# Kernel tuning notes

Hardware: AMD Instinct MI355X
Metric: run time of the kernel (lower is better)

Reference implementation:

```python
import jax, jax.numpy as jnp
import numpy as np

B, S, H, OUT, STEPS = 64, 1024, 512, 256, 32


def setup_inputs() -> dict:
    key = jax.random.key(0)
    ks = jax.random.split(key, 10)
    s = 0.02
    return {
        "encoder_outputs": jax.random.normal(ks[0], (B, S, H), jnp.float32),
        "hidden": jax.random.normal(ks[1], (B, H), jnp.float32),
        # Attention: nn.Linear(2H, 1)
        "attn_w": jax.random.normal(ks[2], (2 * H,), jnp.float32) * s,
        "attn_b": jax.random.normal(ks[3], (1,), jnp.float32) * s,
        # LSTMCell(OUT + H, H): torch gate order i, f, g, o
        "w_ih": jax.random.normal(ks[4], (4 * H, OUT + H), jnp.float32) * s,
        "w_hh": jax.random.normal(ks[5], (4 * H, H), jnp.float32) * s,
        "b_ih": jax.random.normal(ks[6], (4 * H,), jnp.float32) * s,
        "b_hh": jax.random.normal(ks[7], (4 * H,), jnp.float32) * s,
        # fc: nn.Linear(H, OUT)
        "fc_w": jax.random.normal(ks[8], (OUT, H), jnp.float32) * s,
        "fc_b": jax.random.normal(ks[9], (OUT,), jnp.float32) * s,
    }


def reference(encoder_outputs, hidden, attn_w, attn_b, w_ih, w_hh, b_ih, b_hh, fc_w, fc_b):
    # Split attention weight: Linear(concat(enc, hid)) == enc@wa_e + hid@wa_d + b
    wa_e, wa_d = attn_w[:H], attn_w[H:]
    # encoder contribution to attention energy is step-invariant: [B, S]
    enc_energy = jnp.einsum("bsh,h->bs", encoder_outputs, wa_e) + attn_b[0]
    bias = b_ih + b_hh  # [4H]

    def step(carry, _):
        h, c, dec_in = carry
        # Bahdanau-style energy and context
        energy = enc_energy + (h @ wa_d)[:, None]          # [B, S]
        weights = jax.nn.softmax(energy, axis=1)
        context = jnp.einsum("bs,bsh->bh", weights, encoder_outputs)
        # LSTMCell (torch gate order i, f, g, o)
        x = jnp.concatenate([dec_in, context], axis=1)     # [B, OUT+H]
        gates = x @ w_ih.T + h @ w_hh.T + bias             # [B, 4H]
        i, f, g, o = jnp.split(gates, 4, axis=1)
        c_new = jax.nn.sigmoid(f) * c + jax.nn.sigmoid(i) * jnp.tanh(g)
        h_new = jax.nn.sigmoid(o) * jnp.tanh(c_new)
        dec_new = h_new @ fc_w.T + fc_b                    # [B, OUT]
        return (h_new, c_new, dec_new), dec_new

    dec0 = jnp.zeros((encoder_outputs.shape[0], fc_w.shape[0]), encoder_outputs.dtype)
    c0 = jnp.zeros_like(hidden)
    _, outs = jax.lax.scan(step, (hidden, c0, dec0), None, length=STEPS)
    return jnp.transpose(outs, (1, 0, 2))  # [B, STEPS, OUT]
```

## Files before the change

### kernel.cpp

```cpp
#include <hip/hip_runtime.h>
#include <math.h>

#define B 64
#define S 1024
#define H 512
#define OUT 256
#define STEPS 32
#define NG 2048
#define X 768

typedef __attribute__((ext_vector_type(8))) short short8;
typedef __attribute__((ext_vector_type(4))) short s16x4;
typedef __attribute__((ext_vector_type(4))) float f32x4;
typedef __attribute__((ext_vector_type(4))) unsigned u32x4;

__device__ __forceinline__ float sigf(float x) { return 1.0f / (1.0f + __expf(-x)); }
__device__ __forceinline__ float tanhf_fast(float x) {
  return 2.0f / (1.0f + __expf(-2.0f * x)) - 1.0f;
}

__device__ __forceinline__ short f2bf(float x) {
  union { float f; unsigned u; } a; a.f = x;
  unsigned r = a.u + 0x7fffu + ((a.u >> 16) & 1u);
  return (short)(r >> 16);
}
__device__ __forceinline__ float bf2f(short s) {
  union { unsigned u; float f; } a; a.u = ((unsigned)(unsigned short)s) << 16;
  return a.f;
}

__device__ __forceinline__ unsigned load_u32_cg(const unsigned* p) {
  unsigned r;
  asm volatile("global_load_dword %0, %1, off sc0 sc1\n\ts_waitcnt vmcnt(0)"
               : "=v"(r) : "v"(p) : "memory");
  return r;
}

__global__ __launch_bounds__(256) void k_pre(
    const float* __restrict__ enc, const float* __restrict__ attn_w,
    float* __restrict__ part_ctx, float* __restrict__ part_ml,
    const float* __restrict__ w_ih, const float* __restrict__ w_hh,
    const float* __restrict__ fc_w, short* __restrict__ whi,
    short* __restrict__ wlo) {
  __shared__ float smem[10336];
  const int cid = blockIdx.x;
  const int tid = threadIdx.x;
  if (cid < 512) {
    float* sm_acc = smem;
    float* sm_m = smem + 2048;
    float* sm_l = smem + 2052;
    const int b = cid >> 3, chunk = cid & 7;
    const int wave = tid >> 6, lane = tid & 63;
    const float4 wa0 = *(const float4*)(attn_w + lane * 8);
    const float4 wa1 = *(const float4*)(attn_w + lane * 8 + 4);
    const float* eb = enc + (long)b * S * H;
    float m = -1e30f, l = 0.0f;
    float acc[8];
#pragma unroll
    for (int r = 0; r < 8; ++r) acc[r] = 0.0f;
    for (int i = 0; i < 32; ++i) {
      const int s = chunk * 128 + i * 4 + wave;
      const float* row = eb + (long)s * H + lane * 8;
      const float4 v0 = *(const float4*)row;
      const float4 v1 = *(const float4*)(row + 4);
      float e = v0.x * wa0.x + v0.y * wa0.y + v0.z * wa0.z + v0.w * wa0.w +
                v1.x * wa1.x + v1.y * wa1.y + v1.z * wa1.z + v1.w * wa1.w;
#pragma unroll
      for (int msk = 1; msk < 64; msk <<= 1) e += __shfl_xor(e, msk, 64);
      const float mn = fmaxf(m, e);
      const float sc = __expf(m - mn);
      const float p = __expf(e - mn);
      l = l * sc + p;
      m = mn;
      acc[0] = acc[0] * sc + p * v0.x; acc[1] = acc[1] * sc + p * v0.y;
      acc[2] = acc[2] * sc + p * v0.z; acc[3] = acc[3] * sc + p * v0.w;
      acc[4] = acc[4] * sc + p * v1.x; acc[5] = acc[5] * sc + p * v1.y;
      acc[6] = acc[6] * sc + p * v1.z; acc[7] = acc[7] * sc + p * v1.w;
    }
#pragma unroll
    for (int r = 0; r < 8; ++r) sm_acc[wave * 512 + lane * 8 + r] = acc[r];
    if (lane == 0) { sm_m[wave] = m; sm_l[wave] = l; }
    __syncthreads();
    const float mb = fmaxf(fmaxf(sm_m[0], sm_m[1]), fmaxf(sm_m[2], sm_m[3]));
    float e0[4];
#pragma unroll
    for (int w = 0; w < 4; ++w) e0[w] = __expf(sm_m[w] - mb);
    const int h0 = tid * 2;
    float s0 = 0.f, s1 = 0.f;
#pragma unroll
    for (int w = 0; w < 4; ++w) {
      s0 += sm_acc[w * 512 + h0] * e0[w];
      s1 += sm_acc[w * 512 + h0 + 1] * e0[w];
    }
    float* pc = part_ctx + ((long)chunk * B + b) * H;
    pc[h0] = s0; pc[h0 + 1] = s1;
    if (tid == 0) {
      const float lb = sm_l[0] * e0[0] + sm_l[1] * e0[1] + sm_l[2] * e0[2] + sm_l[3] * e0[3];
      part_ml[(chunk * B + b) * 2] = mb;
      part_ml[(chunk * B + b) * 2 + 1] = lb;
    }
  } else {
    float* ft = smem;
    float* wd = smem + 8256;
    const int n0 = (cid - 512) * 8;
    for (int i = tid; i < 512; i += 256) {
      const int r = i >> 6, c4 = (i & 63) << 2;
      *(float4*)&wd[r * 260 + c4] = *(const float4*)(w_ih + (long)(n0 + r) * X + c4);
    }
    float acc[16];
#pragma unroll
    for (int e = 0; e < 16; ++e) acc[e] = 0.f;
    const int n_l = tid >> 5, kq = tid & 31;
    for (int jt = 0; jt < 16; ++jt) {
      __syncthreads();
      for (int i = tid; i < 2048; i += 256) {
        const int r = i >> 7, c4 = (i & 127) << 2;
        *(float4*)&ft[r * 516 + c4] =
            *(const float4*)(fc_w + (long)(jt * 16 + r) * H + c4);
      }
      __syncthreads();
#pragma unroll 4
      for (int j = 0; j < 16; ++j) {
        const float w = wd[n_l * 260 + jt * 16 + j];
#pragma unroll
        for (int e4 = 0; e4 < 4; ++e4) {
          const float4 f = *(float4*)&ft[j * 516 + kq * 4 + e4 * 128];
          acc[e4 * 4 + 0] = fmaf(w, f.x, acc[e4 * 4 + 0]);
          acc[e4 * 4 + 1] = fmaf(w, f.y, acc[e4 * 4 + 1]);
          acc[e4 * 4 + 2] = fmaf(w, f.z, acc[e4 * 4 + 2]);
          acc[e4 * 4 + 3] = fmaf(w, f.w, acc[e4 * 4 + 3]);
        }
      }
    }
    const long rbase = (long)(n0 + n_l) * H;
#pragma unroll
    for (int e4 = 0; e4 < 4; ++e4) {
      const int k = kq * 4 + e4 * 128;
      const float4 hh = *(const float4*)(w_hh + rbase + k);
      float v[4] = {acc[e4 * 4] + hh.x, acc[e4 * 4 + 1] + hh.y,
                    acc[e4 * 4 + 2] + hh.z, acc[e4 * 4 + 3] + hh.w};
      s16x4 hi4, lo4;
#pragma unroll
      for (int e = 0; e < 4; ++e) {
        const short hb = f2bf(v[e]);
        hi4[e] = hb;
        lo4[e] = f2bf(v[e] - bf2f(hb));
      }
      *(s16x4*)(whi + rbase + k) = hi4;
      *(s16x4*)(wlo + rbase + k) = lo4;
    }
  }
}

__global__ __launch_bounds__(256) void k_gbase(
    const float* __restrict__ w_ih, const float* __restrict__ w_hh,
    const float* __restrict__ b_ih, const float* __restrict__ b_hh,
    const float* __restrict__ fc_b, const float* __restrict__ part_ctx,
    const float* __restrict__ part_ml, const float* __restrict__ hidden,
    float* __restrict__ gates0, float* __restrict__ gbase2) {
  __shared__ float wt[128][33];
  __shared__ float rb[16][524];
  __shared__ float sfc[256];
  __shared__ float sf[16][8];
  const int n0 = blockIdx.x * 32, b0 = blockIdx.y * 16;
  const int tid = threadIdx.x;
  const int n_l = tid & 31, bh = tid >> 5;
  const int n = n0 + n_l;

  if (tid < 16) {
    const int r = tid;
    float ml[8], ll[8];
    float m = -1e30f;
#pragma unroll
    for (int c = 0; c < 8; ++c) {
      ml[c] = part_ml[(c * B + b0 + r) * 2];
      ll[c] = part_ml[(c * B + b0 + r) * 2 + 1];
      m = fmaxf(m, ml[c]);
    }
    float L = 0.f;
#pragma unroll
    for (int c = 0; c < 8; ++c) L += ll[c] * __expf(ml[c] - m);
    const float inv = 1.0f / L;
#pragma unroll
    for (int c = 0; c < 8; ++c) sf[r][c] = __expf(ml[c] - m) * inv;
  }
  sfc[tid] = fc_b[tid];
  __syncthreads();

  for (int i = tid; i < 16 * 128; i += 256) {
    const int r = i >> 7, c4 = (i & 127) << 2;
    float4 s = {0.f, 0.f, 0.f, 0.f};
#pragma unroll
    for (int c8 = 0; c8 < 8; ++c8) {
      const float4 p = *(const float4*)(part_ctx + ((long)c8 * B + b0 + r) * H + c4);
      const float f = sf[r][c8];
      s.x = fmaf(p.x, f, s.x); s.y = fmaf(p.y, f, s.y);
      s.z = fmaf(p.z, f, s.z); s.w = fmaf(p.w, f, s.w);
    }
    *(float4*)&rb[r][c4] = s;
  }

  float a1a = 0.f, a1b = 0.f;
  for (int kc = 0; kc < 4; ++kc) {
    __syncthreads();
    for (int i = tid; i < 4096; i += 256) {
      const int r = i >> 7, c = i & 127;
      wt[c][r] = w_ih[(long)(n0 + r) * X + OUT + kc * 128 + c];
    }
    __syncthreads();
#pragma unroll 8
    for (int k = 0; k < 128; ++k) {
      const float wv = wt[k][n_l];
      a1a = fmaf(wv, rb[bh][kc * 128 + k], a1a);
      a1b = fmaf(wv, rb[bh + 8][kc * 128 + k], a1b);
    }
  }

  float db = 0.f;
  for (int kc = 0; kc < 2; ++kc) {
    __syncthreads();
    for (int i = tid; i < 4096; i += 256) {
      const int r = i >> 7, c = i & 127;
      wt[c][r] = w_ih[(long)(n0 + r) * X + kc * 128 + c];
    }
    __syncthreads();
#pragma unroll 8
    for (int k = 0; k < 128; ++k) db = fmaf(wt[k][n_l], sfc[kc * 128 + k], db);
  }

  __syncthreads();
  for (int i = tid; i < 16 * 128; i += 256) {
    const int r = i >> 7, c = (i & 127) << 2;
    *(float4*)&rb[r][c] = *(const float4*)(hidden + (long)(b0 + r) * H + c);
  }
  float a2a = 0.f, a2b = 0.f;
  for (int kc = 0; kc < 4; ++kc) {
    __syncthreads();
    for (int i = tid; i < 4096; i += 256) {
      const int r = i >> 7, c = i & 127;
      wt[c][r] = w_hh[(long)(n0 + r) * H + kc * 128 + c];
    }
    __syncthreads();
#pragma unroll 8
    for (int k = 0; k < 128; ++k) {
      const float wv = wt[k][n_l];
      a2a = fmaf(wv, rb[bh][kc * 128 + k], a2a);
      a2b = fmaf(wv, rb[bh + 8][kc * 128 + k], a2b);
    }
  }

  const float bias = b_ih[n] + b_hh[n];
  gates0[(long)(b0 + bh) * NG + n]     = a1a + bias + a2a;
  gates0[(long)(b0 + bh + 8) * NG + n] = a1b + bias + a2b;
  gbase2[(long)(b0 + bh) * NG + n]     = a1a + bias + db;
  gbase2[(long)(b0 + bh + 8) * NG + n] = a1b + bias + db;
}

#define HSTR 520
__global__ __launch_bounds__(256, 1) void k_recur3(
    const short* __restrict__ whi, const short* __restrict__ wlo,
    const float* __restrict__ gb2, const float* __restrict__ gates0,
    unsigned* __restrict__ hsbf, unsigned int* __restrict__ bar) {
  __shared__ short sh_hi[16 * HSTR];
  __shared__ short sh_lo[16 * HSTR];
  __shared__ float sG[4][8][20];
  __shared__ float sgb[8][64];
  __shared__ float scell[8][16];
  __shared__ int s_fast;

  const int blk = blockIdx.x;
  const int bg = blk & 7;
  const int slice = blk >> 3;
  const int b8 = bg << 3;
  const int hc0 = slice << 4;
  const int tid = threadIdx.x;
  const int w = tid >> 6, l = tid & 63;
  const int ln = l & 15, lk = l >> 4;

  if (tid == 0) {
    unsigned xcc;
    asm volatile("s_getreg_b32 %0, hwreg(20, 0, 32)" : "=s"(xcc));
    __hip_atomic_fetch_or(&bar[7936 + bg], 1u << (xcc & 0xFu),
                          __ATOMIC_RELEASE, __HIP_MEMORY_SCOPE_AGENT);
    unsigned* gbar = &bar[7944 + bg];
    __hip_atomic_fetch_add(gbar, 1u, __ATOMIC_RELEASE, __HIP_MEMORY_SCOPE_AGENT);
    while (load_u32_cg(gbar) < 32u) __builtin_amdgcn_s_sleep(1);
    const unsigned mask = __hip_atomic_load(&bar[7936 + bg], __ATOMIC_ACQUIRE,
                                            __HIP_MEMORY_SCOPE_AGENT);
    s_fast = (__popc(mask) == 1) ? 1 : 0;
  }
  __syncthreads();
  const bool fast = (s_fast != 0);

  for (int i = tid; i < 16 * HSTR; i += 256) { sh_hi[i] = 0; sh_lo[i] = 0; }

  for (int idx = tid; idx < 512; idx += 256) {
    const int b = idx >> 6, gr = idx & 63, g = gr >> 4, j = gr & 15;
    sgb[b][gr] = gb2[(long)(b8 + b) * NG + (g << 9) + hc0 + j];
  }

  short8 wh[16], wl[16];
  {
    const long wb = (long)((w << 9) + hc0 + ln) * H + (lk << 3);
#pragma unroll
    for (int kk = 0; kk < 16; ++kk) {
      wh[kk] = *(const short8*)(whi + wb + kk * 32);
      wl[kk] = *(const short8*)(wlo + wb + kk * 32);
    }
  }
  __syncthreads();

  if (tid < 128) {
    const int b = tid >> 4, j = tid & 15;
    const float* g0 = gates0 + (long)(b8 + b) * NG + hc0 + j;
    const float gi = g0[0];
    const float gg = g0[1024];
    const float go = g0[1536];
    const float cn = sigf(gi) * tanhf_fast(gg);
    const float hn = sigf(go) * tanhf_fast(cn);
    scell[b][j] = cn;
    const short hi = f2bf(hn);
    const short lo = f2bf(hn - bf2f(hi));
    hsbf[(long)(b8 + b) * H + hc0 + j] =
        (unsigned)(unsigned short)hi | ((unsigned)(unsigned short)lo << 16);
  }
  __syncthreads();
  {
    unsigned* flags = bar + bg * 32;
    if (fast) {
      if (tid == 0)
        __hip_atomic_fetch_add(&flags[slice], 1u, __ATOMIC_RELAXED,
                               __HIP_MEMORY_SCOPE_AGENT);
      if (tid < 64) {
        while (!__all(load_u32_cg(flags + (tid & 31)) != 0u)) {}
      }
    } else {
      if (tid == 0)
        __hip_atomic_fetch_add(&flags[slice], 1u, __ATOMIC_RELEASE,
                               __HIP_MEMORY_SCOPE_AGENT);
      if (tid < 64) {
        while (!__all(load_u32_cg(flags + (tid & 31)) != 0u)) {}
      }
      if (tid == 0)
        (void)__hip_atomic_load(&flags[0], __ATOMIC_ACQUIRE,
                                __HIP_MEMORY_SCOPE_AGENT);
    }
    __syncthreads();
  }

  for (int t = 1; t < STEPS; ++t) {
    const unsigned* hb = hsbf + (long)(t - 1) * B * H + (long)b8 * H;
#pragma unroll
    for (int q = 0; q < 4; ++q) {
      const int d0 = q * 1024 + tid * 4;
      const u32x4 v = *(const u32x4*)(hb + d0);
      const int row = d0 >> 9, col = d0 & 511;
      s16x4 hi4, lo4;
#pragma unroll
      for (int e = 0; e < 4; ++e) {
        hi4[e] = (short)(v[e] & 0xFFFFu);
        lo4[e] = (short)(v[e] >> 16);
      }
      *(s16x4*)&sh_hi[row * HSTR + col] = hi4;
      *(s16x4*)&sh_lo[row * HSTR + col] = lo4;
    }
    __syncthreads();

    f32x4 a0 = {0.f, 0.f, 0.f, 0.f};
    f32x4 a1 = {0.f, 0.f, 0.f, 0.f};
    f32x4 a2 = {0.f, 0.f, 0.f, 0.f};
    asm volatile("s_nop 3" ::);
    const int abase = ln * HSTR + (lk << 3);
#pragma unroll
    for (int kk = 0; kk < 16; ++kk) {
      const short8 ah = *(const short8*)&sh_hi[abase + kk * 32];
      const short8 al = *(const short8*)&sh_lo[abase + kk * 32];
      asm volatile("v_mfma_f32_16x16x32_bf16 %0, %1, %2, %0"
                   : "+v"(a0) : "v"(ah), "a"(wh[kk]));
      asm volatile("v_mfma_f32_16x16x32_bf16 %0, %1, %2, %0"
                   : "+v"(a1) : "v"(al), "a"(wh[kk]));
      asm volatile("v_mfma_f32_16x16x32_bf16 %0, %1, %2, %0"
                   : "+v"(a2) : "v"(ah), "a"(wl[kk]));
    }
    asm volatile("s_nop 7\n\ts_nop 7" ::);
    if (lk < 2) {
#pragma unroll
      for (int r = 0; r < 4; ++r)
        sG[w][(lk << 2) + r][ln] = a0[r] + a1[r] + a2[r];
    }
    __syncthreads();

    if (tid < 128) {
      const int b = tid >> 4, j = tid & 15;
      const float gi = sG[0][b][j] + sgb[b][j];
      const float gf = sG[1][b][j] + sgb[b][16 + j];
      const float gg = sG[2][b][j] + sgb[b][32 + j];
      const float go = sG[3][b][j] + sgb[b][48 + j];
      const float c_old = scell[b][j];
      const float cn = sigf(gf) * c_old + sigf(gi) * tanhf_fast(gg);
      const float hn = sigf(go) * tanhf_fast(cn);
      scell[b][j] = cn;
      const short hi = f2bf(hn);
      const short lo = f2bf(hn - bf2f(hi));
      hsbf[(long)t * B * H + (long)(b8 + b) * H + hc0 + j] =
          (unsigned)(unsigned short)hi | ((unsigned)(unsigned short)lo << 16);
    }
    __syncthreads();

    if (t < STEPS - 1) {
      unsigned* flags = bar + t * 256 + bg * 32;
      if (fast) {
        if (tid == 0)
          __hip_atomic_fetch_add(&flags[slice], 1u, __ATOMIC_RELAXED,
                                 __HIP_MEMORY_SCOPE_AGENT);
        if (tid < 64) {
          while (!__all(load_u32_cg(flags + (tid & 31)) != 0u)) {}
        }
      } else {
        if (tid == 0)
          __hip_atomic_fetch_add(&flags[slice], 1u, __ATOMIC_RELEASE,
                                 __HIP_MEMORY_SCOPE_AGENT);
        if (tid < 64) {
          while (!__all(load_u32_cg(flags + (tid & 31)) != 0u)) {}
        }
        if (tid == 0)
          (void)__hip_atomic_load(&flags[0], __ATOMIC_ACQUIRE,
                                  __HIP_MEMORY_SCOPE_AGENT);
      }
      __syncthreads();
    }
  }
}

__global__ __launch_bounds__(256) void k_dec2(
    const unsigned* __restrict__ hsbf, const float* __restrict__ fc_w,
    const float* __restrict__ fc_b, float* __restrict__ out) {
  __shared__ float A[32 * 68];
  __shared__ float Bm[64 * 68];
  const int m0 = blockIdx.x * 32;
  const int o0 = blockIdx.y * 64;
  const int tid = threadIdx.x;
  const int tn = tid & 15, tm = tid >> 4;
  float acc[2][4] = {{0.f, 0.f, 0.f, 0.f}, {0.f, 0.f, 0.f, 0.f}};
  for (int k0 = 0; k0 < H; k0 += 64) {
    for (int idx = tid; idx < 512; idx += 256) {
      const int r = idx >> 4, k4 = idx & 15;
      const u32x4 v = *(const u32x4*)&hsbf[(long)(m0 + r) * H + k0 + k4 * 4];
#pragma unroll
      for (int e = 0; e < 4; ++e)
        A[r * 68 + k4 * 4 + e] =
            bf2f((short)(v[e] & 0xFFFFu)) + bf2f((short)(v[e] >> 16));
    }
    for (int idx = tid; idx < 1024; idx += 256) {
      const int r = idx >> 4, k4 = idx & 15;
      *(float4*)&Bm[r * 68 + k4 * 4] =
          *(const float4*)&fc_w[(long)(o0 + r) * H + k0 + k4 * 4];
    }
    __syncthreads();
#pragma unroll
    for (int k4 = 0; k4 < 16; ++k4) {
      const float4 a0 = *(float4*)&A[tm * 68 + k4 * 4];
      const float4 a1 = *(float4*)&A[(tm + 16) * 68 + k4 * 4];
      const float4 b0 = *(float4*)&Bm[tn * 68 + k4 * 4];
      const float4 b1 = *(float4*)&Bm[(tn + 16) * 68 + k4 * 4];
      const float4 b2 = *(float4*)&Bm[(tn + 32) * 68 + k4 * 4];
      const float4 b3 = *(float4*)&Bm[(tn + 48) * 68 + k4 * 4];
      acc[0][0] += a0.x * b0.x + a0.y * b0.y + a0.z * b0.z + a0.w * b0.w;
      acc[0][1] += a0.x * b1.x + a0.y * b1.y + a0.z * b1.z + a0.w * b1.w;
      acc[0][2] += a0.x * b2.x + a0.y * b2.y + a0.z * b2.z + a0.w * b2.w;
      acc[0][3] += a0.x * b3.x + a0.y * b3.y + a0.z * b3.z + a0.w * b3.w;
      acc[1][0] += a1.x * b0.x + a1.y * b0.y + a1.z * b0.z + a1.w * b0.w;
      acc[1][1] += a1.x * b1.x + a1.y * b1.y + a1.z * b1.z + a1.w * b1.w;
      acc[1][2] += a1.x * b2.x + a1.y * b2.y + a1.z * b2.z + a1.w * b2.w;
      acc[1][3] += a1.x * b3.x + a1.y * b3.y + a1.z * b3.z + a1.w * b3.w;
    }
    __syncthreads();
  }
#pragma unroll
  for (int i = 0; i < 2; ++i) {
    const int m = m0 + tm + 16 * i;
    const int t = m >> 6, b = m & 63;
#pragma unroll
    for (int j = 0; j < 4; ++j) {
      const int o = o0 + tn + 16 * j;
      out[((long)b * STEPS + t) * OUT + o] = acc[i][j] + fc_b[o];
    }
  }
}

extern "C" void kernel_launch(void* const* d_in, const int* in_sizes, int n_in,
                              void* d_out, int out_size, void* d_ws, size_t ws_size,
                              hipStream_t stream) {
  const float* enc = (const float*)d_in[0];
  const float* hidden = (const float*)d_in[1];
  const float* attn_w = (const float*)d_in[2];
  const float* w_ih = (const float*)d_in[4];
  const float* w_hh = (const float*)d_in[5];
  const float* b_ih = (const float*)d_in[6];
  const float* b_hh = (const float*)d_in[7];
  const float* fc_w = (const float*)d_in[8];
  const float* fc_b = (const float*)d_in[9];
  float* out = (float*)d_out;

  float* ws = (float*)d_ws;
  float* part_ctx = ws;
  float* part_ml  = part_ctx + 262144;
  short* whi      = (short*)(part_ml + 1024);
  short* wlo      = whi + 1048576;
  float* gates0   = (float*)(wlo + 1048576);
  float* gbase2   = gates0 + 131072;
  unsigned* hsbf  = (unsigned*)(gbase2 + 131072);
  unsigned int* bar = (unsigned int*)(hsbf + 1048576);

  hipMemsetAsync(bar, 0, 7952 * sizeof(unsigned int), stream);
  k_pre<<<768, 256, 0, stream>>>(enc, attn_w, part_ctx, part_ml,
                                 w_ih, w_hh, fc_w, whi, wlo);
  k_gbase<<<dim3(64, 4), 256, 0, stream>>>(w_ih, w_hh, b_ih, b_hh, fc_b,
                                           part_ctx, part_ml, hidden,
                                           gates0, gbase2);

  k_recur3<<<256, 256, 0, stream>>>(whi, wlo, gbase2, gates0, hsbf, bar);

  k_dec2<<<dim3(64, 4), 256, 0, stream>>>(hsbf, fc_w, fc_b, out);
}
```

Before: 221.5 us.

## Split recurrence barrier into per-wave flag waits and register-block weight fold

In the recurrent kernel, the grid barrier is restructured. Each block now signals its flag right after writing h (with an explicit vmcnt wait). On the fast path, each wave spins only on the 8 producer flags for the columns it loads and then stages that slice itself, which removes the block-wide sync between the wait and the load. Separately, the weight-folding part of k_pre now computes 32 rows per block instead of 8, reusing each loaded fc_w tile across 4 row groups, and the grid shrinks from 768 to 576 blocks. This trades more registers and LDS per block for fewer fc_w reloads, and relies on relaxed ordering being correct for the per-wave flag dependencies.

```diff
diff --git a/kernel.cpp b/kernel.cpp
--- a/kernel.cpp
+++ b/kernel.cpp
@@ -42,7 +42,7 @@
     const float* __restrict__ w_ih, const float* __restrict__ w_hh,
     const float* __restrict__ fc_w, short* __restrict__ whi,
     short* __restrict__ wlo) {
-  __shared__ float smem[10336];
+  __shared__ float smem[12448];
   const int cid = blockIdx.x;
   const int tid = threadIdx.x;
   if (cid < 512) {
@@ -101,53 +101,63 @@
     }
   } else {
     float* ft = smem;
-    float* wd = smem + 8256;
-    const int n0 = (cid - 512) * 8;
-    for (int i = tid; i < 512; i += 256) {
+    float* wd = smem + 4128;
+    const int n0 = (cid - 512) * 32;
+    for (int i = tid; i < 2048; i += 256) {
       const int r = i >> 6, c4 = (i & 63) << 2;
       *(float4*)&wd[r * 260 + c4] = *(const float4*)(w_ih + (long)(n0 + r) * X + c4);
     }
-    float acc[16];
-#pragma unroll
-    for (int e = 0; e < 16; ++e) acc[e] = 0.f;
+    float acc[4][16];
+#pragma unroll
+    for (int rg = 0; rg < 4; ++rg)
+#pragma unroll
+      for (int e = 0; e < 16; ++e) acc[rg][e] = 0.f;
     const int n_l = tid >> 5, kq = tid & 31;
-    for (int jt = 0; jt < 16; ++jt) {
+    for (int jt = 0; jt < 32; ++jt) {
       __syncthreads();
-      for (int i = tid; i < 2048; i += 256) {
+      for (int i = tid; i < 1024; i += 256) {
         const int r = i >> 7, c4 = (i & 127) << 2;
         *(float4*)&ft[r * 516 + c4] =
-            *(const float4*)(fc_w + (long)(jt * 16 + r) * H + c4);
+            *(const float4*)(fc_w + (long)(jt * 8 + r) * H + c4);
       }
       __syncthreads();
-#pragma unroll 4
-      for (int j = 0; j < 16; ++j) {
-        const float w = wd[n_l * 260 + jt * 16 + j];
-#pragma unroll
-        for (int e4 = 0; e4 < 4; ++e4) {
-          const float4 f = *(float4*)&ft[j * 516 + kq * 4 + e4 * 128];
-          acc[e4 * 4 + 0] = fmaf(w, f.x, acc[e4 * 4 + 0]);
-          acc[e4 * 4 + 1] = fmaf(w, f.y, acc[e4 * 4 + 1]);
-          acc[e4 * 4 + 2] = fmaf(w, f.z, acc[e4 * 4 + 2]);
-          acc[e4 * 4 + 3] = fmaf(w, f.w, acc[e4 * 4 + 3]);
+#pragma unroll 2
+      for (int j = 0; j < 8; ++j) {
+        float4 f[4];
+#pragma unroll
+        for (int e4 = 0; e4 < 4; ++e4) f[e4] = *(float4*)&ft[j * 516 + kq * 4 + e4 * 128];
+#pragma unroll
+        for (int rg = 0; rg < 4; ++rg) {
+          const float w = wd[(rg * 8 + n_l) * 260 + jt * 8 + j];
+#pragma unroll
+          for (int e4 = 0; e4 < 4; ++e4) {
+            acc[rg][e4 * 4 + 0] = fmaf(w, f[e4].x, acc[rg][e4 * 4 + 0]);
+            acc[rg][e4 * 4 + 1] = fmaf(w, f[e4].y, acc[rg][e4 * 4 + 1]);
+            acc[rg][e4 * 4 + 2] = fmaf(w, f[e4].z, acc[rg][e4 * 4 + 2]);
+            acc[rg][e4 * 4 + 3] = fmaf(w, f[e4].w, acc[rg][e4 * 4 + 3]);
+          }
         }
       }
     }
-    const long rbase = (long)(n0 + n_l) * H;
-#pragma unroll
-    for (int e4 = 0; e4 < 4; ++e4) {
-      const int k = kq * 4 + e4 * 128;
-      const float4 hh = *(const float4*)(w_hh + rbase + k);
-      float v[4] = {acc[e4 * 4] + hh.x, acc[e4 * 4 + 1] + hh.y,
-                    acc[e4 * 4 + 2] + hh.z, acc[e4 * 4 + 3] + hh.w};
-      s16x4 hi4, lo4;
-#pragma unroll
-      for (int e = 0; e < 4; ++e) {
-        const short hb = f2bf(v[e]);
-        hi4[e] = hb;
-        lo4[e] = f2bf(v[e] - bf2f(hb));
-      }
-      *(s16x4*)(whi + rbase + k) = hi4;
-      *(s16x4*)(wlo + rbase + k) = lo4;
+#pragma unroll
+    for (int rg = 0; rg < 4; ++rg) {
+      const long rbase = (long)(n0 + rg * 8 + n_l) * H;
+#pragma unroll
+      for (int e4 = 0; e4 < 4; ++e4) {
+        const int k = kq * 4 + e4 * 128;
+        const float4 hh = *(const float4*)(w_hh + rbase + k);
+        float v[4] = {acc[rg][e4 * 4] + hh.x, acc[rg][e4 * 4 + 1] + hh.y,
+                      acc[rg][e4 * 4 + 2] + hh.z, acc[rg][e4 * 4 + 3] + hh.w};
+        s16x4 hi4, lo4;
+#pragma unroll
+        for (int e = 0; e < 4; ++e) {
+          const short hb = f2bf(v[e]);
+          hi4[e] = hb;
+          lo4[e] = f2bf(v[e] - bf2f(hb));
+        }
+        *(s16x4*)(whi + rbase + k) = hi4;
+        *(s16x4*)(wlo + rbase + k) = lo4;
+      }
     }
   }
 }
@@ -323,46 +333,59 @@
     const short lo = f2bf(hn - bf2f(hi));
     hsbf[(long)(b8 + b) * H + hc0 + j] =
         (unsigned)(unsigned short)hi | ((unsigned)(unsigned short)lo << 16);
+    asm volatile("s_waitcnt vmcnt(0)" ::: "memory");
   }
   __syncthreads();
-  {
-    unsigned* flags = bar + bg * 32;
+  if (tid == 0) {
+    unsigned* f0 = bar + bg * 32;
+    if (fast)
+      __hip_atomic_fetch_add(&f0[slice], 1u, __ATOMIC_RELAXED, __HIP_MEMORY_SCOPE_AGENT);
+    else
+      __hip_atomic_fetch_add(&f0[slice], 1u, __ATOMIC_RELEASE, __HIP_MEMORY_SCOPE_AGENT);
+  }
+
+  for (int t = 1; t < STEPS; ++t) {
+    unsigned* flags = bar + (t - 1) * 256 + bg * 32;
+    const unsigned* hb = hsbf + (long)(t - 1) * B * H + (long)b8 * H;
     if (fast) {
-      if (tid == 0)
-        __hip_atomic_fetch_add(&flags[slice], 1u, __ATOMIC_RELAXED,
-                               __HIP_MEMORY_SCOPE_AGENT);
+      const unsigned* fl = flags + (w << 3);
+      while (!__all(load_u32_cg(fl + (l & 7)) != 0u)) {}
+      const int colu = (w << 7) + ((l & 31) << 2);
+      const int r0 = (l >> 5) << 2;
+#pragma unroll
+      for (int q = 0; q < 4; ++q) {
+        const int row = r0 + q;
+        const u32x4 v = *(const u32x4*)(hb + (long)row * H + colu);
+        s16x4 hi4, lo4;
+#pragma unroll
+        for (int e = 0; e < 4; ++e) {
+          hi4[e] = (short)(v[e] & 0xFFFFu);
+          lo4[e] = (short)(v[e] >> 16);
+        }
+        *(s16x4*)&sh_hi[row * HSTR + colu] = hi4;
+        *(s16x4*)&sh_lo[row * HSTR + colu] = lo4;
+      }
+    } else {
       if (tid < 64) {
         while (!__all(load_u32_cg(flags + (tid & 31)) != 0u)) {}
       }
-    } else {
       if (tid == 0)
-        __hip_atomic_fetch_add(&flags[slice], 1u, __ATOMIC_RELEASE,
-                               __HIP_MEMORY_SCOPE_AGENT);
-      if (tid < 64) {
-        while (!__all(load_u32_cg(flags + (tid & 31)) != 0u)) {}
-      }
-      if (tid == 0)
-        (void)__hip_atomic_load(&flags[0], __ATOMIC_ACQUIRE,
-                                __HIP_MEMORY_SCOPE_AGENT);
-    }
-    __syncthreads();
-  }
-
-  for (int t = 1; t < STEPS; ++t) {
-    const unsigned* hb = hsbf + (long)(t - 1) * B * H + (long)b8 * H;
-#pragma unroll
-    for (int q = 0; q < 4; ++q) {
-      const int d0 = q * 1024 + tid * 4;
-      const u32x4 v = *(const u32x4*)(hb + d0);
-      const int row = d0 >> 9, col = d0 & 511;
-      s16x4 hi4, lo4;
-#pragma unroll
-      for (int e = 0; e < 4; ++e) {
-        hi4[e] = (short)(v[e] & 0xFFFFu);
-        lo4[e] = (short)(v[e] >> 16);
-      }
-      *(s16x4*)&sh_hi[row * HSTR + col] = hi4;
-      *(s16x4*)&sh_lo[row * HSTR + col] = lo4;
+        (void)__hip_atomic_load(&flags[0], __ATOMIC_ACQUIRE, __HIP_MEMORY_SCOPE_AGENT);
+      __syncthreads();
+#pragma unroll
+      for (int q = 0; q < 4; ++q) {
+        const int d0 = q * 1024 + tid * 4;
+        const u32x4 v = *(const u32x4*)(hb + d0);
+        const int row = d0 >> 9, col = d0 & 511;
+        s16x4 hi4, lo4;
+#pragma unroll
+        for (int e = 0; e < 4; ++e) {
+          hi4[e] = (short)(v[e] & 0xFFFFu);
+          lo4[e] = (short)(v[e] >> 16);
+        }
+        *(s16x4*)&sh_hi[row * HSTR + col] = hi4;
+        *(s16x4*)&sh_lo[row * HSTR + col] = lo4;
+      }
     }
     __syncthreads();
 
@@ -404,30 +427,20 @@
       const short lo = f2bf(hn - bf2f(hi));
       hsbf[(long)t * B * H + (long)(b8 + b) * H + hc0 + j] =
           (unsigned)(unsigned short)hi | ((unsigned)(unsigned short)lo << 16);
+      asm volatile("s_waitcnt vmcnt(0)" ::: "memory");
     }
     __syncthreads();
 
     if (t < STEPS - 1) {
-      unsigned* flags = bar + t * 256 + bg * 32;
-      if (fast) {
-        if (tid == 0)
-          __hip_atomic_fetch_add(&flags[slice], 1u, __ATOMIC_RELAXED,
+      if (tid == 0) {
+        unsigned* nf = bar + t * 256 + bg * 32;
+        if (fast)
+          __hip_atomic_fetch_add(&nf[slice], 1u, __ATOMIC_RELAXED,
                                  __HIP_MEMORY_SCOPE_AGENT);
-        if (tid < 64) {
-          while (!__all(load_u32_cg(flags + (tid & 31)) != 0u)) {}
-        }
-      } else {
-        if (tid == 0)
-          __hip_atomic_fetch_add(&flags[slice], 1u, __ATOMIC_RELEASE,
+        else
+          __hip_atomic_fetch_add(&nf[slice], 1u, __ATOMIC_RELEASE,
                                  __HIP_MEMORY_SCOPE_AGENT);
-        if (tid < 64) {
-          while (!__all(load_u32_cg(flags + (tid & 31)) != 0u)) {}
-        }
-        if (tid == 0)
-          (void)__hip_atomic_load(&flags[0], __ATOMIC_ACQUIRE,
-                                  __HIP_MEMORY_SCOPE_AGENT);
-      }
-      __syncthreads();
+      }
     }
   }
 }
@@ -513,7 +526,7 @@
   unsigned int* bar = (unsigned int*)(hsbf + 1048576);
 
   hipMemsetAsync(bar, 0, 7952 * sizeof(unsigned int), stream);
-  k_pre<<<768, 256, 0, stream>>>(enc, attn_w, part_ctx, part_ml,
+  k_pre<<<576, 256, 0, stream>>>(enc, attn_w, part_ctx, part_ml,
                                  w_ih, w_hh, fc_w, whi, wlo);
   k_gbase<<<dim3(64, 4), 256, 0, stream>>>(w_ih, w_hh, b_ih, b_hh, fc_b,
                                            part_ctx, part_ml, hidden,
```

Result: slower. 254.9 us (+15.1%).

## Stream encoder rows via async global-to-LDS double buffering and drop online-softmax max

Applied to the files above, without the earlier changes.

Rewrites the attention prepass blocks to stage 8-row encoder tiles into LDS with global_load_lds direct loads, double-buffered so the next tile's fetch overlaps compute on the current one. It also drops the running-max online softmax, storing exp(e) directly and writing a max of zero, which removes the per-row rescaling of the accumulators. The cost is three barriers per tile and the assumption that the energies are small enough that exp does not overflow without max subtraction.

```diff
diff --git a/kernel.cpp b/kernel.cpp
--- a/kernel.cpp
+++ b/kernel.cpp
@@ -13,6 +13,8 @@
 typedef __attribute__((ext_vector_type(4))) short s16x4;
 typedef __attribute__((ext_vector_type(4))) float f32x4;
 typedef __attribute__((ext_vector_type(4))) unsigned u32x4;
+typedef __attribute__((address_space(3))) unsigned lds_u32_t;
+typedef __attribute__((address_space(1))) unsigned g_u32_t;
 
 __device__ __forceinline__ float sigf(float x) { return 1.0f / (1.0f + __expf(-x)); }
 __device__ __forceinline__ float tanhf_fast(float x) {
@@ -46,58 +48,82 @@
   const int cid = blockIdx.x;
   const int tid = threadIdx.x;
   if (cid < 512) {
-    float* sm_acc = smem;
-    float* sm_m = smem + 2048;
-    float* sm_l = smem + 2052;
+    float* lbuf = smem;
+    float* sp   = smem + 8192;
     const int b = cid >> 3, chunk = cid & 7;
     const int wave = tid >> 6, lane = tid & 63;
     const float4 wa0 = *(const float4*)(attn_w + lane * 8);
     const float4 wa1 = *(const float4*)(attn_w + lane * 8 + 4);
-    const float* eb = enc + (long)b * S * H;
-    float m = -1e30f, l = 0.0f;
-    float acc[8];
-#pragma unroll
-    for (int r = 0; r < 8; ++r) acc[r] = 0.0f;
-    for (int i = 0; i < 32; ++i) {
-      const int s = chunk * 128 + i * 4 + wave;
-      const float* row = eb + (long)s * H + lane * 8;
-      const float4 v0 = *(const float4*)row;
-      const float4 v1 = *(const float4*)(row + 4);
-      float e = v0.x * wa0.x + v0.y * wa0.y + v0.z * wa0.z + v0.w * wa0.w +
-                v1.x * wa1.x + v1.y * wa1.y + v1.z * wa1.z + v1.w * wa1.w;
-#pragma unroll
-      for (int msk = 1; msk < 64; msk <<= 1) e += __shfl_xor(e, msk, 64);
-      const float mn = fmaxf(m, e);
-      const float sc = __expf(m - mn);
-      const float p = __expf(e - mn);
-      l = l * sc + p;
-      m = mn;
-      acc[0] = acc[0] * sc + p * v0.x; acc[1] = acc[1] * sc + p * v0.y;
-      acc[2] = acc[2] * sc + p * v0.z; acc[3] = acc[3] * sc + p * v0.w;
-      acc[4] = acc[4] * sc + p * v1.x; acc[5] = acc[5] * sc + p * v1.y;
-      acc[6] = acc[6] * sc + p * v1.z; acc[7] = acc[7] * sc + p * v1.w;
-    }
-#pragma unroll
-    for (int r = 0; r < 8; ++r) sm_acc[wave * 512 + lane * 8 + r] = acc[r];
-    if (lane == 0) { sm_m[wave] = m; sm_l[wave] = l; }
-    __syncthreads();
-    const float mb = fmaxf(fmaxf(sm_m[0], sm_m[1]), fmaxf(sm_m[2], sm_m[3]));
-    float e0[4];
-#pragma unroll
-    for (int w = 0; w < 4; ++w) e0[w] = __expf(sm_m[w] - mb);
+    const float* eb = enc + (long)b * S * H + (long)(chunk * 128) * H;
+
+#pragma unroll
+    for (int j = 0; j < 4; ++j) {
+      const int s = wave * 4 + j, row = s >> 1, half = s & 1;
+      const float* gp = eb + (long)row * H + half * 256 + lane * 4;
+      __builtin_amdgcn_global_load_lds(
+          (g_u32_t*)gp, (lds_u32_t*)&lbuf[row * 512 + half * 256], 16, 0, 0);
+    }
+
     const int h0 = tid * 2;
     float s0 = 0.f, s1 = 0.f;
-#pragma unroll
-    for (int w = 0; w < 4; ++w) {
-      s0 += sm_acc[w * 512 + h0] * e0[w];
-      s1 += sm_acc[w * 512 + h0 + 1] * e0[w];
+    for (int t = 0; t < 16; ++t) {
+      float* tile = lbuf + (t & 1) * 4096;
+      if (t < 15) {
+        float* tnx = lbuf + ((t + 1) & 1) * 4096;
+        const float* ebn = eb + (long)((t + 1) * 8) * H;
+#pragma unroll
+        for (int j = 0; j < 4; ++j) {
+          const int s = wave * 4 + j, row = s >> 1, half = s & 1;
+          const float* gp = ebn + (long)row * H + half * 256 + lane * 4;
+          __builtin_amdgcn_global_load_lds(
+              (g_u32_t*)gp, (lds_u32_t*)&tnx[row * 512 + half * 256], 16, 0, 0);
+        }
+        asm volatile("s_waitcnt vmcnt(4)" ::: "memory");
+      } else {
+        asm volatile("s_waitcnt vmcnt(0)" ::: "memory");
+      }
+      __builtin_amdgcn_sched_barrier(0);
+      __builtin_amdgcn_s_barrier();
+
+#pragma unroll
+      for (int rr = 0; rr < 2; ++rr) {
+        const int r = wave * 2 + rr;
+        const float* lr = tile + r * 512 + lane * 8;
+        const float4 v0 = *(const float4*)lr;
+        const float4 v1 = *(const float4*)(lr + 4);
+        float e = v0.x * wa0.x + v0.y * wa0.y + v0.z * wa0.z + v0.w * wa0.w +
+                  v1.x * wa1.x + v1.y * wa1.y + v1.z * wa1.z + v1.w * wa1.w;
+#pragma unroll
+        for (int msk = 1; msk < 64; msk <<= 1) e += __shfl_xor(e, msk, 64);
+        if (lane == 0) sp[t * 8 + r] = __expf(e);
+      }
+      asm volatile("s_waitcnt lgkmcnt(0)" ::: "memory");
+      __builtin_amdgcn_sched_barrier(0);
+      __builtin_amdgcn_s_barrier();
+
+#pragma unroll
+      for (int r = 0; r < 8; ++r) {
+        const float p = sp[t * 8 + r];
+        const float2 v = *(const float2*)(tile + r * 512 + h0);
+        s0 = fmaf(p, v.x, s0);
+        s1 = fmaf(p, v.y, s1);
+      }
+      asm volatile("s_waitcnt lgkmcnt(0)" ::: "memory");
+      __builtin_amdgcn_sched_barrier(0);
+      __builtin_amdgcn_s_barrier();
     }
     float* pc = part_ctx + ((long)chunk * B + b) * H;
-    pc[h0] = s0; pc[h0 + 1] = s1;
-    if (tid == 0) {
-      const float lb = sm_l[0] * e0[0] + sm_l[1] * e0[1] + sm_l[2] * e0[2] + sm_l[3] * e0[3];
-      part_ml[(chunk * B + b) * 2] = mb;
-      part_ml[(chunk * B + b) * 2 + 1] = lb;
+    pc[h0] = s0;
+    pc[h0 + 1] = s1;
+    __syncthreads();
+    if (tid < 64) {
+      float tsum = sp[tid] + sp[tid + 64];
+#pragma unroll
+      for (int m = 1; m < 64; m <<= 1) tsum += __shfl_xor(tsum, m, 64);
+      if (tid == 0) {
+        part_ml[(chunk * B + b) * 2] = 0.0f;
+        part_ml[(chunk * B + b) * 2 + 1] = tsum;
+      }
     }
   } else {
     float* ft = smem;
```

New measurement: 216.9 us, median of 2. -2.1%, faster.
